# Kernel optimization log

Measured on AMD Instinct MI355X. Metric: run time of the kernel, lower is better.

## Reference

```python
import jax, jax.numpy as jnp
import numpy as np

D = 384      # d_model
H = 6        # num_heads
K = 8        # k_neighbors
B = 8        # batch
N = 2048     # num points
EPS = 1e-5


def _layer_norm(x, g, b):
    m = jnp.mean(x, axis=-1, keepdims=True)
    v = jnp.var(x, axis=-1, keepdims=True)
    return (x - m) * jax.lax.rsqrt(v + EPS) * g + b


def setup_inputs() -> dict:
    key = jax.random.key(0)
    ks = jax.random.split(key, 12)
    s = 0.02
    return {
        "coords": jax.random.normal(ks[0], (B, 3, N), jnp.float32),
        "features": jax.random.normal(ks[1], (B, D, N), jnp.float32),
        "ln1_g": jnp.ones((D,), jnp.float32),
        "ln1_b": jnp.zeros((D,), jnp.float32),
        "w_qkv": jax.random.normal(ks[2], (D, 3 * D), jnp.float32) * s,
        "w_attn_out": jax.random.normal(ks[3], (D, D), jnp.float32) * s,
        "b_attn_out": jnp.zeros((D,), jnp.float32),
        "ga_wq": jax.random.normal(ks[4], (D, D), jnp.float32) * s,
        "ga_wk": jax.random.normal(ks[5], (D, D), jnp.float32) * s,
        "ga_wv": jax.random.normal(ks[6], (D, D), jnp.float32) * s,
        "merge_w": jax.random.normal(ks[7], (2 * D, D), jnp.float32) * s,
        "merge_b": jnp.zeros((D,), jnp.float32),
        "ln2_g": jnp.ones((D,), jnp.float32),
        "ln2_b": jnp.zeros((D,), jnp.float32),
        "ff_w1": jax.random.normal(ks[8], (D, 2 * D), jnp.float32) * s,
        "ff_b1": jnp.zeros((2 * D,), jnp.float32),
        "ff_w2": jax.random.normal(ks[9], (2 * D, D), jnp.float32) * s,
        "ff_b2": jnp.zeros((D,), jnp.float32),
    }


def reference(coords, features, ln1_g, ln1_b, w_qkv, w_attn_out, b_attn_out,
              ga_wq, ga_wk, ga_wv, merge_w, merge_b, ln2_g, ln2_b,
              ff_w1, ff_b1, ff_w2, ff_b2):
    b, d, n = features.shape
    dh = d // H
    f = jnp.swapaxes(features, 1, 2)          # [B, N, D]
    nf = _layer_norm(f, ln1_g, ln1_b)         # [B, N, D]

    # --- dense multi-head self-attention branch ---
    qkv = nf @ w_qkv                           # [B, N, 3D]
    q, k, v = jnp.split(qkv, 3, axis=-1)
    def heads(x):
        return x.reshape(b, n, H, dh).transpose(0, 2, 1, 3)  # [B, H, N, dh]
    scores = jnp.einsum('bhqd,bhkd->bhqk', heads(q), heads(k)) / jnp.sqrt(jnp.float32(dh))
    attn = jnp.einsum('bhqk,bhkd->bhqd', jax.nn.softmax(scores, axis=-1), heads(v))
    attn = attn.transpose(0, 2, 1, 3).reshape(b, n, d)
    attn = attn @ w_attn_out + b_attn_out      # output projection

    # --- KNN graph-attention branch over normalized features ---
    c = jnp.swapaxes(coords, 1, 2)             # [B, N, 3]
    sq = jnp.sum(c * c, axis=-1)               # [B, N]
    d2 = sq[:, :, None] + sq[:, None, :] - 2.0 * jnp.einsum('bnd,bmd->bnm', c, c)
    _, idx = jax.lax.top_k(-d2, K)             # [B, N, K] nearest-neighbor indices
    nbrs = jax.vmap(lambda fe, i: fe[i])(nf, idx)  # [B, N, K, D]
    gq = nf @ ga_wq                             # [B, N, D]
    gk = nbrs @ ga_wk                           # [B, N, K, D]
    gv = nbrs @ ga_wv
    gs = jnp.einsum('bnd,bnkd->bnk', gq, gk) / jnp.sqrt(jnp.float32(d))
    geom = jnp.einsum('bnk,bnkd->bnd', jax.nn.softmax(gs, axis=-1), gv)  # [B, N, D]

    # --- merge + residual + FFN ---
    merged = jnp.concatenate([attn, geom], axis=-1) @ merge_w + merge_b
    f = f + merged
    h = _layer_norm(f, ln2_g, ln2_b)
    f = f + (jax.nn.gelu(h @ ff_w1 + ff_b1) @ ff_w2 + ff_b2)
    return jnp.swapaxes(f, 1, 2)               # [B, D, N]
```

## Files before the change

kernel.cpp:

```cpp
#include <hip/hip_runtime.h>
#include <hip/hip_bf16.h>
#include <cstdint>

#define D_MODEL 384
#define NHEAD 6
#define DHEAD 64
#define NPTS 2048
#define BATCH 8

typedef __attribute__((ext_vector_type(8))) short short8;
typedef __attribute__((ext_vector_type(4))) float floatx4;
typedef __attribute__((ext_vector_type(2))) unsigned int u32x2;
typedef __attribute__((ext_vector_type(4))) unsigned int u32x4;

__device__ __forceinline__ float bf2f(unsigned short u) {
    return __uint_as_float(((unsigned int)u) << 16);
}

__device__ __forceinline__ unsigned short f2bf(float f) {
    unsigned int u = __float_as_uint(f);
    unsigned int r = (u + 0x7FFFu + ((u >> 16) & 1u)) >> 16;
    return (unsigned short)r;
}

__device__ __forceinline__ unsigned cvtpk(float lo, float hi) {
    unsigned r;
    asm("v_cvt_pk_bf16_f32 %0, %1, %2" : "=v"(r) : "v"(lo), "v"(hi));
    return r;
}

#define TR16(dst, addr, imm) \
    asm volatile("ds_read_b64_tr_b16 %0, %1 offset:" #imm : "=v"(dst) : "v"(addr))

__device__ __forceinline__ float gelu_tanh(float x) {
    float x3 = x * x * x;
    return 0.5f * x * (1.0f + tanhf(0.7978845608028654f * (x + 0.044715f * x3)));
}

__device__ __forceinline__ void gload_lds16(const unsigned short* g, unsigned short* l) {
    __builtin_amdgcn_global_load_lds(
        (const __attribute__((address_space(1))) unsigned int*)g,
        (__attribute__((address_space(3))) unsigned int*)l, 16, 0, 0);
}

__global__ __launch_bounds__(256) void k_wprep(
    const float* __restrict__ wqkv, const float* __restrict__ wao,
    const float* __restrict__ wq, const float* __restrict__ wk,
    const float* __restrict__ wv, const float* __restrict__ wm,
    const float* __restrict__ w1, const float* __restrict__ w2,
    unsigned short* __restrict__ qkvT, unsigned short* __restrict__ aoT,
    unsigned short* __restrict__ gaT, unsigned short* __restrict__ mT,
    unsigned short* __restrict__ f1T, unsigned short* __restrict__ f2T) {
    __shared__ float tile[32][33];
    int id = blockIdx.x;
    const float* src;
    unsigned short* dst;
    int K, N;
    if (id < 432)       {            src = wqkv; dst = qkvT;            K = 384; N = 1152; }
    else if (id < 576)  { id -= 432; src = wao;  dst = aoT;             K = 384; N = 384; }
    else if (id < 720)  { id -= 576; src = wq;   dst = gaT;             K = 384; N = 384; }
    else if (id < 864)  { id -= 720; src = wk;   dst = gaT + 384 * 384; K = 384; N = 384; }
    else if (id < 1008) { id -= 864; src = wv;   dst = gaT + 768 * 384; K = 384; N = 384; }
    else if (id < 1296) { id -= 1008; src = wm;  dst = mT;              K = 768; N = 384; }
    else if (id < 1584) { id -= 1296; src = w1;  dst = f1T;             K = 384; N = 768; }
    else                { id -= 1584; src = w2;  dst = f2T;             K = 768; N = 384; }
    int ntiles = N >> 5;
    int nt = id % ntiles, kt = id / ntiles;
    int tx = threadIdx.x, ty = threadIdx.y;
#pragma unroll
    for (int i = 0; i < 32; i += 8)
        tile[ty + i][tx] = src[(size_t)(kt * 32 + ty + i) * N + nt * 32 + tx];
    __syncthreads();
#pragma unroll
    for (int i = 0; i < 32; i += 8)
        dst[(size_t)(nt * 32 + ty + i) * K + kt * 32 + tx] = f2bf(tile[tx][ty + i]);
}

__global__ __launch_bounds__(256) void k_transpose_in(const float* __restrict__ feat,
                                                      unsigned short* __restrict__ f) {
    __shared__ float tile[32][33];
    int b = blockIdx.z;
    int n0 = blockIdx.x * 32, d0 = blockIdx.y * 32;
    int tx = threadIdx.x, ty = threadIdx.y;
#pragma unroll
    for (int i = 0; i < 32; i += 8)
        tile[ty + i][tx] = feat[((size_t)b * D_MODEL + d0 + ty + i) * NPTS + n0 + tx];
    __syncthreads();
#pragma unroll
    for (int i = 0; i < 32; i += 8)
        f[((size_t)b * NPTS + n0 + ty + i) * D_MODEL + d0 + tx] = f2bf(tile[tx][ty + i]);
}

__global__ __launch_bounds__(256) void k_transpose_out(const unsigned short* __restrict__ f,
                                                       float* __restrict__ out) {
    __shared__ float tile[32][33];
    int b = blockIdx.z;
    int d0 = blockIdx.x * 32, n0 = blockIdx.y * 32;
    int tx = threadIdx.x, ty = threadIdx.y;
#pragma unroll
    for (int i = 0; i < 32; i += 8)
        tile[ty + i][tx] = bf2f(f[((size_t)b * NPTS + n0 + ty + i) * D_MODEL + d0 + tx]);
    __syncthreads();
#pragma unroll
    for (int i = 0; i < 32; i += 8)
        out[((size_t)b * D_MODEL + d0 + ty + i) * NPTS + n0 + tx] = tile[tx][ty + i];
}

__global__ __launch_bounds__(256) void k_vt(const unsigned short* __restrict__ qkv,
                                            unsigned short* __restrict__ vt) {
    __shared__ unsigned short tile[32][33];
    int b = blockIdx.z;
    int h = blockIdx.y >> 1, d0 = (blockIdx.y & 1) * 32;
    int n0 = blockIdx.x * 32;
    int tx = threadIdx.x, ty = threadIdx.y;
#pragma unroll
    for (int i = 0; i < 32; i += 8)
        tile[ty + i][tx] =
            qkv[((size_t)b * NPTS + n0 + ty + i) * 1152 + 768 + h * 64 + d0 + tx];
    __syncthreads();
#pragma unroll
    for (int i = 0; i < 32; i += 8)
        vt[(((size_t)(b * NHEAD + h) * 64) + d0 + ty + i) * NPTS + n0 + tx] = tile[tx][ty + i];
}

__global__ __launch_bounds__(128) void k_layernorm(const unsigned short* __restrict__ x,
                                                   const float* __restrict__ g,
                                                   const float* __restrict__ bt,
                                                   unsigned short* __restrict__ y) {
    int row = blockIdx.x, t = threadIdx.x;
    const unsigned short* xr = x + (size_t)row * D_MODEL;
    float v0 = bf2f(xr[t]), v1 = bf2f(xr[t + 128]), v2 = bf2f(xr[t + 256]);
    float s = v0 + v1 + v2;
    float s2 = v0 * v0 + v1 * v1 + v2 * v2;
#pragma unroll
    for (int off = 32; off > 0; off >>= 1) {
        s += __shfl_xor(s, off, 64);
        s2 += __shfl_xor(s2, off, 64);
    }
    __shared__ float ps[2], ps2[2];
    if ((t & 63) == 0) { ps[t >> 6] = s; ps2[t >> 6] = s2; }
    __syncthreads();
    s = ps[0] + ps[1];
    s2 = ps2[0] + ps2[1];
    float mean = s * (1.0f / 384.0f);
    float var = s2 * (1.0f / 384.0f) - mean * mean;
    var = fmaxf(var, 0.0f);
    float inv = 1.0f / sqrtf(var + 1e-5f);
    unsigned short* yr = y + (size_t)row * D_MODEL;
    yr[t]       = f2bf((v0 - mean) * inv * g[t]       + bt[t]);
    yr[t + 128] = f2bf((v1 - mean) * inv * g[t + 128] + bt[t + 128]);
    yr[t + 256] = f2bf((v2 - mean) * inv * g[t + 256] + bt[t + 256]);
}

__global__ __launch_bounds__(256) void k_knn(const float* __restrict__ coords,
                                             int* __restrict__ idx) {
    __shared__ float4 cpts[NPTS];
    int b = blockIdx.x >> 9;
    int q0 = (blockIdx.x & 511) * 4;
    const float* cb = coords + (size_t)b * 3 * NPTS;
    int tid = threadIdx.x;
#pragma unroll
    for (int i = 0; i < 8; i++) {
        int m = tid + i * 256;
        float x = cb[m], y = cb[NPTS + m], z = cb[2 * NPTS + m];
        float sq = __fadd_rn(__fadd_rn(__fmul_rn(x, x), __fmul_rn(y, y)), __fmul_rn(z, z));
        cpts[m] = make_float4(x, y, z, sq);
    }
    __syncthreads();
    int wv = tid >> 6, lane = tid & 63;
    int n = q0 + wv;
    float4 qp = cpts[n];
    float qx = qp.x, qy = qp.y, qz = qp.z, sqn = qp.w;
    unsigned long long heap[8];
#pragma unroll
    for (int k = 0; k < 8; k++) heap[k] = 0xFFFFFFFFFFFFFFFFull;
    for (int j = 0; j < 32; j++) {
        int m = j * 64 + lane;
        float4 cp = cpts[m];
        float dot = __fadd_rn(__fadd_rn(__fmul_rn(qx, cp.x), __fmul_rn(qy, cp.y)),
                              __fmul_rn(qz, cp.z));
        float d2 = __fsub_rn(__fadd_rn(sqn, cp.w), __fmul_rn(2.0f, dot));
        unsigned int u = __float_as_uint(d2);
        u = (u & 0x80000000u) ? ~u : (u | 0x80000000u);
        unsigned long long key = ((unsigned long long)u << 32) | (unsigned int)m;
        if (key < heap[7]) {
            unsigned long long cur = key;
#pragma unroll
            for (int t2 = 0; t2 < 8; t2++) {
                unsigned long long h = heap[t2];
                unsigned long long lo = h < cur ? h : cur;
                cur = h < cur ? cur : h;
                heap[t2] = lo;
            }
        }
    }
    unsigned long long cur = heap[0];
    unsigned int out[8];
#pragma unroll
    for (int r = 0; r < 8; r++) {
        unsigned long long w = cur;
#pragma unroll
        for (int off = 1; off < 64; off <<= 1) {
            unsigned long long o = __shfl_xor(w, off, 64);
            w = o < w ? o : w;
        }
        out[r] = (unsigned int)(w & 0xFFFFFFFFu);
        if (cur == w) {
#pragma unroll
            for (int t2 = 0; t2 < 7; t2++) heap[t2] = heap[t2 + 1];
            heap[7] = 0xFFFFFFFFFFFFFFFFull;
            cur = heap[0];
        }
    }
    if (lane == 0) {
        unsigned int* outr = (unsigned int*)(idx + ((size_t)b * NPTS + n) * 8);
        *(uint4*)outr = make_uint4(out[0], out[1], out[2], out[3]);
        *(uint4*)(outr + 4) = make_uint4(out[4], out[5], out[6], out[7]);
    }
}

__global__ __launch_bounds__(256) void k_gemm(const unsigned short* __restrict__ A, int lda,
                                              const unsigned short* __restrict__ WT,
                                              const float* __restrict__ bias,
                                              const unsigned short* __restrict__ res,
                                              unsigned short* __restrict__ C, int ldc,
                                              int K, int act) {
    __shared__ unsigned short Alds[2 * 128 * 32];
    __shared__ unsigned short Wlds[2 * 128 * 32];
    int tid = threadIdx.x;
    int wv = tid >> 6, lane = tid & 63;
    int l15 = lane & 15, quad = lane >> 4;
    int row0 = blockIdx.y * 128, col0 = blockIdx.x * 128;
    int wm = wv >> 1, wn = wv & 1;
    int wbase = tid & 192;
    floatx4 acc[4][4];
#pragma unroll
    for (int i = 0; i < 4; i++)
#pragma unroll
        for (int j = 0; j < 4; j++) acc[i][j] = (floatx4){0.f, 0.f, 0.f, 0.f};
    for (int k0 = 0; k0 < K; k0 += 64) {
#pragma unroll
        for (int i = 0; i < 4; i++) {
            int idx = i * 256 + tid;
            int kc = idx >> 9, row = (idx >> 2) & 127, ko = idx & 3;
            unsigned short* ldst = Alds + (size_t)(i * 256 + wbase) * 8;
            gload_lds16(A + (size_t)(row0 + row) * lda + k0 + kc * 32 + ko * 8, ldst);
            unsigned short* ldstw = Wlds + (size_t)(i * 256 + wbase) * 8;
            gload_lds16(WT + (size_t)(col0 + row) * K + k0 + kc * 32 + ko * 8, ldstw);
        }
        __syncthreads();
#pragma unroll
        for (int kc = 0; kc < 2; kc++) {
            short8 af[4], bf[4];
#pragma unroll
            for (int i = 0; i < 4; i++)
                af[i] = *(const short8*)&Alds[kc * 4096 + (wm * 64 + i * 16 + l15) * 32 + quad * 8];
#pragma unroll
            for (int j = 0; j < 4; j++)
                bf[j] = *(const short8*)&Wlds[kc * 4096 + (wn * 64 + j * 16 + l15) * 32 + quad * 8];
#pragma unroll
            for (int i = 0; i < 4; i++)
#pragma unroll
                for (int j = 0; j < 4; j++)
                    acc[i][j] =
                        __builtin_amdgcn_mfma_f32_16x16x32_bf16(bf[j], af[i], acc[i][j], 0, 0, 0);
        }
        __syncthreads();
    }
#pragma unroll
    for (int i = 0; i < 4; i++) {
        int r = row0 + wm * 64 + i * 16 + l15;
#pragma unroll
        for (int j = 0; j < 4; j++) {
            int cb = col0 + wn * 64 + j * 16 + quad * 4;
            float4 bv = bias ? *(const float4*)(bias + cb) : make_float4(0.f, 0.f, 0.f, 0.f);
            float v0 = acc[i][j][0] + bv.x;
            float v1 = acc[i][j][1] + bv.y;
            float v2 = acc[i][j][2] + bv.z;
            float v3 = acc[i][j][3] + bv.w;
            if (act == 1) {
                v0 = gelu_tanh(v0); v1 = gelu_tanh(v1);
                v2 = gelu_tanh(v2); v3 = gelu_tanh(v3);
            }
            if (res) {
                uint2 rv = *(const uint2*)(res + (size_t)r * ldc + cb);
                const unsigned short* rs = (const unsigned short*)&rv;
                v0 += bf2f(rs[0]); v1 += bf2f(rs[1]);
                v2 += bf2f(rs[2]); v3 += bf2f(rs[3]);
            }
            ushort4 u;
            u.x = f2bf(v0); u.y = f2bf(v1); u.z = f2bf(v2); u.w = f2bf(v3);
            *(ushort4*)(C + (size_t)r * ldc + cb) = u;
        }
    }
}

__global__ __launch_bounds__(256, 3) void k_attn(const unsigned short* __restrict__ qkv,
                                                 const unsigned short* __restrict__ vt,
                                                 unsigned short* __restrict__ attn) {
    __shared__ unsigned short Klds[2][64 * 64];
    __shared__ unsigned short VTl[2][64 * 64];
    __shared__ unsigned short Pt[4][2048];
    int b = blockIdx.z, h = blockIdx.y;
    int tid = threadIdx.x;
    int wv = tid >> 6, lane = tid & 63;
    int l15 = lane & 15, quad = lane >> 4;
    int qbase = blockIdx.x * 128 + wv * 32;
    const unsigned short* qkvb = qkv + (size_t)b * NPTS * 1152;
    const unsigned short* vtb = vt + (size_t)(b * NHEAD + h) * 64 * NPTS;
    const float SC = 0.18033688011112042f;
    short8 qf[2][2];
#pragma unroll
    for (int qt = 0; qt < 2; qt++) {
        const unsigned short* qptr =
            qkvb + (size_t)(qbase + qt * 16 + l15) * 1152 + h * 64 + quad * 8;
        qf[qt][0] = *(const short8*)qptr;
        qf[qt][1] = *(const short8*)(qptr + 32);
#pragma unroll
        for (int g = 0; g < 2; g++) {
            short8 v = qf[qt][g];
#pragma unroll
            for (int e = 0; e < 8; e++)
                v[e] = (short)f2bf(bf2f((unsigned short)v[e]) * SC);
            qf[qt][g] = v;
        }
    }
    short8 ones;
#pragma unroll
    for (int e = 0; e < 8; e++) ones[e] = (short)0x3F80;
    int x7 = l15 & 7;
    int sk0 = ((quad ^ x7) << 4);
    int sk1 = (((quad + 4) ^ x7) << 4);
    unsigned pa = (unsigned)(size_t)(__attribute__((address_space(3))) unsigned short*)&Pt[wv][0] +
                  (unsigned)(quad * 256 + l15 * 2);
    int sdg = tid & 7;
    floatx4 o[2][4];
#pragma unroll
    for (int qt = 0; qt < 2; qt++)
#pragma unroll
        for (int ct = 0; ct < 4; ct++) o[qt][ct] = (floatx4){0.f, 0.f, 0.f, 0.f};
    floatx4 l4[2];
    l4[0] = (floatx4){0.f, 0.f, 0.f, 0.f};
    l4[1] = (floatx4){0.f, 0.f, 0.f, 0.f};

    auto stage = [&](int c, int k0) {
#pragma unroll
        for (int i = 0; i < 2; i++) {
            int id = i * 256 + tid;
            int row = id >> 3;
            int sl = sdg ^ (row & 7);
            gload_lds16(qkvb + (size_t)(k0 + row) * 1152 + 384 + h * 64 + sl * 8,
                        &Klds[c][(size_t)(i * 256 + (tid & 192)) * 8]);
            gload_lds16(vtb + (size_t)row * NPTS + k0 + sl * 8,
                        &VTl[c][(size_t)(i * 256 + (tid & 192)) * 8]);
        }
    };

    stage(0, 0);
    __syncthreads();
    for (int t = 0; t < 32; ++t) {
        int c = t & 1;
        if (t < 31) stage(c ^ 1, (t + 1) * 64);
        const char* Kb = (const char*)&Klds[c][0];
        const char* Vb = (const char*)&VTl[c][0];
        short8 kf[4][2];
#pragma unroll
        for (int ct = 0; ct < 4; ct++) {
            kf[ct][0] = *(const short8*)(Kb + (ct * 16 + l15) * 128 + sk0);
            kf[ct][1] = *(const short8*)(Kb + (ct * 16 + l15) * 128 + sk1);
        }
#pragma unroll
        for (int qt = 0; qt < 2; qt++) {
            floatx4 s4[4];
#pragma unroll
            for (int ct = 0; ct < 4; ct++) {
                floatx4 z = (floatx4){0.f, 0.f, 0.f, 0.f};
                z = __builtin_amdgcn_mfma_f32_16x16x32_bf16(qf[qt][0], kf[ct][0], z, 0, 0, 0);
                z = __builtin_amdgcn_mfma_f32_16x16x32_bf16(qf[qt][1], kf[ct][1], z, 0, 0, 0);
                s4[ct] = z;
            }
#pragma unroll
            for (int ct = 0; ct < 4; ct++) {
                float p0 = __builtin_amdgcn_exp2f(s4[ct][0]);
                float p1 = __builtin_amdgcn_exp2f(s4[ct][1]);
                float p2 = __builtin_amdgcn_exp2f(s4[ct][2]);
                float p3 = __builtin_amdgcn_exp2f(s4[ct][3]);
                u32x2 pk;
                pk.x = cvtpk(p0, p1);
                pk.y = cvtpk(p2, p3);
                *(u32x2*)&Pt[wv][qt * 1024 + (ct * 16 + l15) * 16 + quad * 4] = pk;
            }
        }
        short8 vf[4][2];
#pragma unroll
        for (int ct = 0; ct < 4; ct++) {
            vf[ct][0] = *(const short8*)(Vb + (ct * 16 + l15) * 128 + sk0);
            vf[ct][1] = *(const short8*)(Vb + (ct * 16 + l15) * 128 + sk1);
        }
        asm volatile("s_waitcnt lgkmcnt(0)" ::: "memory");
        u32x2 q0g0l, q0g0h, q0g1l, q0g1h, q1g0l, q1g0h, q1g1l, q1g1h;
        TR16(q0g0l, pa, 0);
        TR16(q0g0h, pa, 128);
        TR16(q0g1l, pa, 1024);
        TR16(q0g1h, pa, 1152);
        TR16(q1g0l, pa, 2048);
        TR16(q1g0h, pa, 2176);
        TR16(q1g1l, pa, 3072);
        TR16(q1g1h, pa, 3200);
        asm volatile("s_waitcnt lgkmcnt(0)" ::: "memory");
        __builtin_amdgcn_sched_barrier(0);
        short8 pf[2][2];
        pf[0][0] = __builtin_bit_cast(short8, (u32x4){q0g0l.x, q0g0l.y, q0g0h.x, q0g0h.y});
        pf[0][1] = __builtin_bit_cast(short8, (u32x4){q0g1l.x, q0g1l.y, q0g1h.x, q0g1h.y});
        pf[1][0] = __builtin_bit_cast(short8, (u32x4){q1g0l.x, q1g0l.y, q1g0h.x, q1g0h.y});
        pf[1][1] = __builtin_bit_cast(short8, (u32x4){q1g1l.x, q1g1l.y, q1g1h.x, q1g1h.y});
#pragma unroll
        for (int ct = 0; ct < 4; ct++) {
#pragma unroll
            for (int qt = 0; qt < 2; qt++) {
                o[qt][ct] = __builtin_amdgcn_mfma_f32_16x16x32_bf16(vf[ct][0], pf[qt][0], o[qt][ct], 0, 0, 0);
                o[qt][ct] = __builtin_amdgcn_mfma_f32_16x16x32_bf16(vf[ct][1], pf[qt][1], o[qt][ct], 0, 0, 0);
            }
        }
#pragma unroll
        for (int qt = 0; qt < 2; qt++) {
            l4[qt] = __builtin_amdgcn_mfma_f32_16x16x32_bf16(ones, pf[qt][0], l4[qt], 0, 0, 0);
            l4[qt] = __builtin_amdgcn_mfma_f32_16x16x32_bf16(ones, pf[qt][1], l4[qt], 0, 0, 0);
        }
        if (t < 31) __syncthreads();
    }
#pragma unroll
    for (int qt = 0; qt < 2; qt++) {
        float linv = 1.0f / l4[qt][0];
#pragma unroll
        for (int ct = 0; ct < 4; ct++) {
            ushort4 u;
            u.x = f2bf(o[qt][ct][0] * linv);
            u.y = f2bf(o[qt][ct][1] * linv);
            u.z = f2bf(o[qt][ct][2] * linv);
            u.w = f2bf(o[qt][ct][3] * linv);
            *(ushort4*)(attn + ((size_t)b * NPTS + qbase + qt * 16 + l15) * 384 + h * 64 +
                        ct * 16 + quad * 4) = u;
        }
    }
}

__global__ __launch_bounds__(64) void k_geom(const unsigned short* __restrict__ gap,
                                             const int* __restrict__ idx,
                                             unsigned short* __restrict__ cat) {
    int r = blockIdx.x;
    int b = r >> 11;
    int t = threadIdx.x;
    int nb[8];
#pragma unroll
    for (int k = 0; k < 8; k++) nb[k] = idx[(size_t)r * 8 + k];
    const unsigned short* gqr = gap + (size_t)r * 1152;
    float qv[6];
#pragma unroll
    for (int j = 0; j < 6; j++) qv[j] = bf2f(gqr[t + 64 * j]);
    float s[8];
#pragma unroll
    for (int k = 0; k < 8; k++) {
        const unsigned short* nkr = gap + ((size_t)b * NPTS + nb[k]) * 1152 + 384;
        float acc = 0.0f;
#pragma unroll
        for (int j = 0; j < 6; j++) acc += qv[j] * bf2f(nkr[t + 64 * j]);
#pragma unroll
        for (int mm = 32; mm > 0; mm >>= 1) acc += __shfl_xor(acc, mm, 64);
        s[k] = acc * 0.05103103630798287f;
    }
    float mx = s[0];
#pragma unroll
    for (int k = 1; k < 8; k++) mx = fmaxf(mx, s[k]);
    float w[8];
    float sum = 0.0f;
#pragma unroll
    for (int k = 0; k < 8; k++) { w[k] = __expf(s[k] - mx); sum += w[k]; }
    float inv = 1.0f / sum;
    unsigned short* outr = cat + (size_t)r * 768 + 384;
#pragma unroll
    for (int j = 0; j < 6; j++) {
        int d = t + 64 * j;
        float acc = 0.0f;
#pragma unroll
        for (int k = 0; k < 8; k++)
            acc += w[k] * bf2f(gap[((size_t)b * NPTS + nb[k]) * 1152 + 768 + d]);
        outr[d] = f2bf(acc * inv);
    }
}

extern "C" void kernel_launch(void* const* d_in, const int* in_sizes, int n_in,
                              void* d_out, int out_size, void* d_ws, size_t ws_size,
                              hipStream_t stream) {
    (void)in_sizes; (void)n_in; (void)out_size; (void)ws_size;
    const float* coords     = (const float*)d_in[0];
    const float* features   = (const float*)d_in[1];
    const float* ln1_g      = (const float*)d_in[2];
    const float* ln1_b      = (const float*)d_in[3];
    const float* w_qkv      = (const float*)d_in[4];
    const float* w_attn_out = (const float*)d_in[5];
    const float* b_attn_out = (const float*)d_in[6];
    const float* ga_wq      = (const float*)d_in[7];
    const float* ga_wk      = (const float*)d_in[8];
    const float* ga_wv      = (const float*)d_in[9];
    const float* merge_w    = (const float*)d_in[10];
    const float* merge_b    = (const float*)d_in[11];
    const float* ln2_g      = (const float*)d_in[12];
    const float* ln2_b      = (const float*)d_in[13];
    const float* ff_w1      = (const float*)d_in[14];
    const float* ff_b1      = (const float*)d_in[15];
    const float* ff_w2      = (const float*)d_in[16];
    const float* ff_b2      = (const float*)d_in[17];

    unsigned short* W0 = (unsigned short*)d_ws;
    const size_t SZ = (size_t)BATCH * NPTS * D_MODEL;
    unsigned short* F    = W0 + 0 * SZ;
    unsigned short* NF   = W0 + 1 * SZ;
    unsigned short* QKV  = W0 + 2 * SZ;
    unsigned short* ATTN = W0 + 5 * SZ;
    unsigned short* VT   = W0 + 6 * SZ;
    unsigned short* CAT  = W0 + 2 * SZ;
    unsigned short* GAP  = W0 + 4 * SZ;
    unsigned short* F2   = W0 + 4 * SZ;
    unsigned short* HB   = W0 + 1 * SZ;
    unsigned short* T1   = W0 + 5 * SZ;
    unsigned short* FFIN = W0 + 2 * SZ;
    int*            IDX  = (int*)(W0 + 7 * SZ);
    unsigned short* WTS  = W0 + 7 * SZ + 262144;
    unsigned short* qkvT = WTS;
    unsigned short* aoT  = qkvT + 442368;
    unsigned short* gaT  = aoT + 147456;
    unsigned short* mT   = gaT + 442368;
    unsigned short* f1T  = mT + 294912;
    unsigned short* f2T  = f1T + 294912;

    const int M = BATCH * NPTS;

    k_wprep<<<1872, dim3(32, 8), 0, stream>>>(w_qkv, w_attn_out, ga_wq, ga_wk, ga_wv,
                                              merge_w, ff_w1, ff_w2,
                                              qkvT, aoT, gaT, mT, f1T, f2T);
    k_transpose_in<<<dim3(NPTS / 32, D_MODEL / 32, BATCH), dim3(32, 8), 0, stream>>>(features, F);
    k_layernorm<<<M, 128, 0, stream>>>(F, ln1_g, ln1_b, NF);
    k_knn<<<BATCH * (NPTS / 4), 256, 0, stream>>>(coords, IDX);
    k_gemm<<<dim3(9, M / 128), 256, 0, stream>>>(NF, 384, qkvT, nullptr, nullptr,
                                                 QKV, 1152, 384, 0);
    k_vt<<<dim3(NPTS / 32, 2 * NHEAD, BATCH), dim3(32, 8), 0, stream>>>(QKV, VT);
    k_attn<<<dim3(NPTS / 128, NHEAD, BATCH), 256, 0, stream>>>(QKV, VT, ATTN);
    k_gemm<<<dim3(3, M / 128), 256, 0, stream>>>(ATTN, 384, aoT, b_attn_out, nullptr,
                                                 CAT, 768, 384, 0);
    k_gemm<<<dim3(9, M / 128), 256, 0, stream>>>(NF, 384, gaT, nullptr, nullptr,
                                                 GAP, 1152, 384, 0);
    k_geom<<<M, 64, 0, stream>>>(GAP, IDX, CAT);
    k_gemm<<<dim3(3, M / 128), 256, 0, stream>>>(CAT, 768, mT, merge_b, F,
                                                 F2, 384, 768, 0);
    k_layernorm<<<M, 128, 0, stream>>>(F2, ln2_g, ln2_b, HB);
    k_gemm<<<dim3(6, M / 128), 256, 0, stream>>>(HB, 384, f1T, ff_b1, nullptr,
                                                 T1, 768, 384, 1);
    k_gemm<<<dim3(3, M / 128), 256, 0, stream>>>(T1, 768, f2T, ff_b2, F2,
                                                 FFIN, 384, 768, 0);
    k_transpose_out<<<dim3(D_MODEL / 32, NPTS / 32, BATCH), dim3(32, 8), 0, stream>>>(
        FFIN, (float*)d_out);
}
```

Measured before the change: 480.7 us.

## Use 32-bit distance keys with threshold-based KNN index extraction

The KNN top-k kernel now keeps a branchless per-lane top-8 of 32-bit distance keys instead of 64-bit key|index pairs, and caches all 32 keys per lane in registers. The cross-lane reduction runs only on 32-bit values to find the 8th-smallest distance. A second pass then uses ballot and popcount compaction to write the indices strictly below that threshold, and breaks ties by lowest index. This halves the shuffle and compare width, at the cost of more registers and an extra scan. The output order becomes lane/j order rather than sorted by distance, which only matters if later code depends on that order.

New measurement: 447.5 us. -6.9%, faster.

```diff
diff --git a/kernel.cpp b/kernel.cpp
--- a/kernel.cpp
+++ b/kernel.cpp
@@ -171,51 +171,82 @@
     int n = q0 + wv;
     float4 qp = cpts[n];
     float qx = qp.x, qy = qp.y, qz = qp.z, sqn = qp.w;
-    unsigned long long heap[8];
-#pragma unroll
-    for (int k = 0; k < 8; k++) heap[k] = 0xFFFFFFFFFFFFFFFFull;
+    unsigned keys[32];
+    unsigned h[8];
+#pragma unroll
+    for (int k = 0; k < 8; k++) h[k] = 0xFFFFFFFFu;
+#pragma unroll
     for (int j = 0; j < 32; j++) {
-        int m = j * 64 + lane;
-        float4 cp = cpts[m];
+        float4 cp = cpts[j * 64 + lane];
         float dot = __fadd_rn(__fadd_rn(__fmul_rn(qx, cp.x), __fmul_rn(qy, cp.y)),
                               __fmul_rn(qz, cp.z));
         float d2 = __fsub_rn(__fadd_rn(sqn, cp.w), __fmul_rn(2.0f, dot));
-        unsigned int u = __float_as_uint(d2);
-        u = (u & 0x80000000u) ? ~u : (u | 0x80000000u);
-        unsigned long long key = ((unsigned long long)u << 32) | (unsigned int)m;
-        if (key < heap[7]) {
-            unsigned long long cur = key;
-#pragma unroll
-            for (int t2 = 0; t2 < 8; t2++) {
-                unsigned long long h = heap[t2];
-                unsigned long long lo = h < cur ? h : cur;
-                cur = h < cur ? cur : h;
-                heap[t2] = lo;
-            }
-        }
-    }
-    unsigned long long cur = heap[0];
-    unsigned int out[8];
+        unsigned u = __float_as_uint(d2);
+        u ^= (unsigned)(((int)u >> 31)) | 0x80000000u;
+        keys[j] = u;
+        unsigned cur = u;
+#pragma unroll
+        for (int t2 = 0; t2 < 8; t2++) {
+            unsigned lo = h[t2] < cur ? h[t2] : cur;
+            cur = h[t2] < cur ? cur : h[t2];
+            h[t2] = lo;
+        }
+    }
+    unsigned curh = h[0];
+    unsigned T8 = 0;
 #pragma unroll
     for (int r = 0; r < 8; r++) {
-        unsigned long long w = cur;
+        unsigned w = curh;
 #pragma unroll
         for (int off = 1; off < 64; off <<= 1) {
-            unsigned long long o = __shfl_xor(w, off, 64);
+            unsigned o = __shfl_xor(w, off, 64);
             w = o < w ? o : w;
         }
-        out[r] = (unsigned int)(w & 0xFFFFFFFFu);
-        if (cur == w) {
-#pragma unroll
-            for (int t2 = 0; t2 < 7; t2++) heap[t2] = heap[t2 + 1];
-            heap[7] = 0xFFFFFFFFFFFFFFFFull;
-            cur = heap[0];
-        }
-    }
-    if (lane == 0) {
-        unsigned int* outr = (unsigned int*)(idx + ((size_t)b * NPTS + n) * 8);
-        *(uint4*)outr = make_uint4(out[0], out[1], out[2], out[3]);
-        *(uint4*)(outr + 4) = make_uint4(out[4], out[5], out[6], out[7]);
+        T8 = w;
+        if (r < 7) {
+            unsigned long long mask = __ballot(curh == w);
+            if (curh == w && (mask & ((1ull << lane) - 1ull)) == 0) {
+#pragma unroll
+                for (int t2 = 0; t2 < 7; t2++) h[t2] = h[t2 + 1];
+                h[7] = 0xFFFFFFFFu;
+                curh = h[0];
+            }
+        }
+    }
+    int* outr = idx + ((size_t)b * NPTS + n) * 8;
+    int cnt = 0;
+    unsigned meq = 0xFFFFFFFFu;
+#pragma unroll
+    for (int j = 0; j < 32; j++) {
+        unsigned m = (unsigned)(j * 64 + lane);
+        bool strict = keys[j] < T8;
+        unsigned long long msk = __ballot(strict);
+        if (strict) {
+            int pos = cnt + (int)__popcll(msk & ((1ull << lane) - 1ull));
+            outr[pos] = (int)m;
+        }
+        cnt += (int)__popcll(msk);
+        if (keys[j] == T8 && m < meq) meq = m;
+    }
+    while (cnt < 8) {
+        unsigned w = meq;
+#pragma unroll
+        for (int off = 1; off < 64; off <<= 1) {
+            unsigned o = __shfl_xor(w, off, 64);
+            w = o < w ? o : w;
+        }
+        bool winner = (meq == w);
+        if (winner) outr[cnt] = (int)w;
+        cnt++;
+        if (cnt >= 8) break;
+        if (winner) {
+            meq = 0xFFFFFFFFu;
+#pragma unroll
+            for (int j = 0; j < 32; j++) {
+                unsigned m = (unsigned)(j * 64 + lane);
+                if (keys[j] == T8 && m > w && m < meq) meq = m;
+            }
+        }
     }
 }
 
```
